# Kernel optimization log

Measured on AMD Instinct MI355X. Metric: run time of the kernel, lower is better.

The kernel has to match this reference:

```python
import jax, jax.numpy as jnp
import numpy as np

HID = 2880
NQ = 64
NKV = 8
HD = 64
THETA = 150000.0
WINDOW = 128
S = 8192


def _rope(x, positions):
    # x: [S, H, D]; half-split (rotate_half) convention
    d = x.shape[-1]
    inv_freq = 1.0 / (THETA ** (jnp.arange(0, d, 2, dtype=jnp.float32) / d))  # [D/2]
    ang = positions.astype(jnp.float32)[:, None] * inv_freq[None, :]          # [S, D/2]
    cos = jnp.cos(ang)[:, None, :]
    sin = jnp.sin(ang)[:, None, :]
    x1, x2 = jnp.split(x, 2, axis=-1)
    return jnp.concatenate([x1 * cos - x2 * sin, x2 * cos + x1 * sin], axis=-1)


def setup_inputs() -> dict:
    key = jax.random.key(0)
    ks = jax.random.split(key, 12)
    sd = 0.02
    return {
        "hidden": jax.random.normal(ks[0], (S, HID), dtype=jnp.float32),
        "positions": jnp.arange(S, dtype=jnp.int64) if jax.config.jax_enable_x64 else jnp.arange(S, dtype=jnp.int32),
        "Wq": jax.random.normal(ks[1], (HID, NQ * HD), dtype=jnp.float32) * sd,
        "bq": jax.random.normal(ks[2], (NQ * HD,), dtype=jnp.float32) * sd,
        "Wk": jax.random.normal(ks[3], (HID, NKV * HD), dtype=jnp.float32) * sd,
        "bk": jax.random.normal(ks[4], (NKV * HD,), dtype=jnp.float32) * sd,
        "Wv": jax.random.normal(ks[5], (HID, NKV * HD), dtype=jnp.float32) * sd,
        "bv": jax.random.normal(ks[6], (NKV * HD,), dtype=jnp.float32) * sd,
        "Wo": jax.random.normal(ks[7], (NQ * HD, HID), dtype=jnp.float32) * sd,
        "bo": jax.random.normal(ks[8], (HID,), dtype=jnp.float32) * sd,
    }


def _attention(hidden, positions, Wq, bq, Wk, bk, Wv, bv, Wo, bo):
    n_tok = hidden.shape[0]
    q = (hidden @ Wq + bq).reshape(n_tok, NQ, HD)
    k = (hidden @ Wk + bk).reshape(n_tok, NKV, HD)
    v = (hidden @ Wv + bv).reshape(n_tok, NKV, HD)
    q = _rope(q, positions)
    k = _rope(k, positions)

    # Blocked sliding-window causal attention (window == block size W).
    W = WINDOW
    nb = n_tok // W
    group = NQ // NKV
    qb = q.reshape(nb, W, NQ, HD)
    kb = k.reshape(nb, W, NKV, HD)
    vb = v.reshape(nb, W, NKV, HD)
    # each query block attends to its own block plus the previous one (2W keys)
    k_prev = jnp.concatenate([jnp.zeros_like(kb[:1]), kb[:-1]], axis=0)
    v_prev = jnp.concatenate([jnp.zeros_like(vb[:1]), vb[:-1]], axis=0)
    k_ctx = jnp.concatenate([k_prev, kb], axis=1)   # [nb, 2W, NKV, HD]
    v_ctx = jnp.concatenate([v_prev, vb], axis=1)
    # GQA: repeat KV heads to match query heads
    k_ctx = jnp.repeat(k_ctx, group, axis=2)        # [nb, 2W, NQ, HD]
    v_ctx = jnp.repeat(v_ctx, group, axis=2)

    scale = 1.0 / np.sqrt(HD)
    scores = jnp.einsum('bqhd,bkhd->bhqk', qb, k_ctx) * scale  # [nb, NQ, W, 2W]

    qi = jnp.arange(W)[:, None]            # local query pos
    ki = jnp.arange(2 * W)[None, :]        # local key pos within context
    diff = qi - ki + W                     # i - j (global)
    band = (diff >= 0) & (diff < WINDOW)   # causal + window
    kpos = jnp.arange(nb)[:, None, None] * W + ki[None] - W  # global key pos
    mask = band[None] & (kpos >= 0)        # [nb, W, 2W]

    neg = jnp.finfo(scores.dtype).min
    scores = jnp.where(mask[:, None, :, :], scores, neg)
    p = jax.nn.softmax(scores, axis=-1)
    attn = jnp.einsum('bhqk,bkhd->bqhd', p, v_ctx)  # [nb, W, NQ, HD]
    attn = attn.reshape(n_tok, NQ * HD)
    return attn @ Wo + bo


def reference(hidden, positions, Wq, bq, Wk, bk, Wv, bv, Wo, bo):
    return _attention(hidden, positions, Wq, bq, Wk, bk, Wv, bv, Wo, bo)
```

## Files before the change

### kernel.cpp

```cpp
#include <hip/hip_runtime.h>
#include <stdint.h>

#define S_TOK 8192
#define HID 2880
#define NQ 64
#define NKV 8
#define HD 64
#define QKV_N 5120
#define NO_PAD 2944

typedef __attribute__((ext_vector_type(8))) __bf16 bf16x8;
typedef __attribute__((ext_vector_type(4))) float f32x4;

__device__ __forceinline__ unsigned short f2bf(float f) {
  unsigned int u = __builtin_bit_cast(unsigned int, f);
  u += 0x7fff + ((u >> 16) & 1);
  return (unsigned short)(u >> 16);
}
__device__ __forceinline__ float bf2f(unsigned short h) {
  unsigned int u = ((unsigned int)h) << 16;
  return __builtin_bit_cast(float, u);
}

__device__ __forceinline__ void async_lds16(const void* g, void* l) {
  __builtin_amdgcn_global_load_lds(
      (const __attribute__((address_space(1))) unsigned int*)g,
      (__attribute__((address_space(3))) unsigned int*)l, 16, 0, 0);
}

__device__ __forceinline__ void wg_barrier() {
  asm volatile("" ::: "memory");
  __builtin_amdgcn_s_barrier();
  asm volatile("" ::: "memory");
}

__global__ __launch_bounds__(256) void cvt_bf16_kernel(
    const float* __restrict__ src, unsigned short* __restrict__ dst) {
  size_t i = ((size_t)blockIdx.x * 256 + threadIdx.x) * 8;
  float4 a = *(const float4*)(src + i);
  float4 b = *(const float4*)(src + i + 4);
  union { unsigned short u[8]; uint4 v; } o;
  o.u[0] = f2bf(a.x); o.u[1] = f2bf(a.y); o.u[2] = f2bf(a.z); o.u[3] = f2bf(a.w);
  o.u[4] = f2bf(b.x); o.u[5] = f2bf(b.y); o.u[6] = f2bf(b.z); o.u[7] = f2bf(b.w);
  *(uint4*)(dst + i) = o.v;
}

__global__ __launch_bounds__(256) void transpose_cvt(
    const float* __restrict__ src, unsigned short* __restrict__ dst,
    int R, int C, int rowOff) {
  __shared__ float tile[32][33];
  int tx = threadIdx.x, ty = threadIdx.y;
  int c0 = blockIdx.x * 32, r0 = blockIdx.y * 32;
#pragma unroll
  for (int i = 0; i < 4; ++i)
    tile[ty + i * 8][tx] = src[(size_t)(r0 + ty + i * 8) * C + c0 + tx];
  __syncthreads();
#pragma unroll
  for (int i = 0; i < 4; ++i)
    dst[(size_t)(c0 + ty + i * 8 + rowOff) * R + r0 + tx] = f2bf(tile[tx][ty + i * 8]);
}

__global__ __launch_bounds__(256) void rope_kernel(
    unsigned short* __restrict__ qkv, const int* __restrict__ positions) {
  int gid = blockIdx.x * 256 + threadIdx.x;
  int d = gid & 31;
  int rest = gid >> 5;
  int head = rest % 72;
  int t = rest / 72;
  unsigned short* p = qkv + (size_t)t * QKV_N + head * 64;
  float x1 = bf2f(p[d]);
  float x2 = bf2f(p[d + 32]);
  float pos = (float)positions[t];
  float inv = exp2f(-0.5373313430f * (float)d);
  float ang = pos * inv;
  float s = sinf(ang), c = cosf(ang);
  p[d] = f2bf(x1 * c - x2 * s);
  p[d + 32] = f2bf(x2 * c + x1 * s);
}

template <int MODE>
__global__ __launch_bounds__(512, 2) void gemm256(
    const unsigned short* __restrict__ A, const unsigned short* __restrict__ BT,
    void* __restrict__ Cout, int K, int NT,
    const float* __restrict__ b0, const float* __restrict__ b1,
    const float* __restrict__ b2) {
  __shared__ unsigned short lds[3 * 24576];
  const int tid = threadIdx.x;
  const int lane = tid & 63;
  const int wid = tid >> 6;
  const int wy = wid >> 2, wx = wid & 3;
  const int l15 = lane & 15, l4 = lane >> 4;
  const int m0 = blockIdx.y * 256, n0 = blockIdx.x * 128;

  const unsigned short* Ag = A + (size_t)m0 * K;
  const unsigned short* Bg = BT + (size_t)n0 * K;

  f32x4 acc[8][2];
#pragma unroll
  for (int m = 0; m < 8; ++m)
#pragma unroll
    for (int n = 0; n < 2; ++n)
#pragma unroll
      for (int r = 0; r < 4; ++r) acc[m][n][r] = 0.f;

  auto stageA = [&](int t, int buf) {
    unsigned short* dst = lds + buf * 24576;
    const unsigned short* G = Ag + t * 64;
#pragma unroll
    for (int rd = 0; rd < 4; ++rd) {
      int s = tid + rd * 512;
      int row = s >> 3;
      int g = (s & 7) ^ (row & 7);
      async_lds16(G + (size_t)row * K + g * 8, &dst[s * 8]);
    }
  };
  auto stageB = [&](int t, int buf) {
    unsigned short* dst = lds + buf * 24576 + 16384;
    const unsigned short* G = Bg + t * 64;
#pragma unroll
    for (int rd = 0; rd < 2; ++rd) {
      int s = tid + rd * 512;
      int row = s >> 3;
      int g = (s & 7) ^ (row & 7);
      async_lds16(G + (size_t)row * K + g * 8, &dst[s * 8]);
    }
  };

  stageA(0, 0); stageB(0, 0);
  stageA(1, 1); stageB(1, 1);
  asm volatile("s_waitcnt vmcnt(6)" ::: "memory");
  wg_barrier();

  int cur = 0, nxt = 2;
  for (int t = 0; t < NT; ++t) {
    const unsigned short* As = lds + cur * 24576;
    const unsigned short* Bs = As + 16384;
    bf16x8 bfrag[2][2], af0[4][2], af1[4][2];

#pragma unroll
    for (int n = 0; n < 2; ++n)
#pragma unroll
      for (int ks = 0; ks < 2; ++ks) {
        int row = wx * 32 + n * 16 + l15;
        int ch = (ks * 4 + l4) ^ (row & 7);
        bfrag[n][ks] = *(const bf16x8*)&Bs[row * 64 + ch * 8];
      }
#pragma unroll
    for (int m = 0; m < 4; ++m)
#pragma unroll
      for (int ks = 0; ks < 2; ++ks) {
        int row = wy * 128 + m * 16 + l15;
        int ch = (ks * 4 + l4) ^ (row & 7);
        af0[m][ks] = *(const bf16x8*)&As[row * 64 + ch * 8];
      }
    if (t + 2 < NT) stageA(t + 2, nxt);
    wg_barrier();
    asm volatile("s_waitcnt lgkmcnt(0)" ::: "memory");
    __builtin_amdgcn_sched_barrier(0);
    __builtin_amdgcn_s_setprio(1);
#pragma unroll
    for (int m = 0; m < 4; ++m)
#pragma unroll
      for (int n = 0; n < 2; ++n)
#pragma unroll
        for (int ks = 0; ks < 2; ++ks)
          acc[m][n] = __builtin_amdgcn_mfma_f32_16x16x32_bf16(
              af0[m][ks], bfrag[n][ks], acc[m][n], 0, 0, 0);
    __builtin_amdgcn_s_setprio(0);
    wg_barrier();

#pragma unroll
    for (int m = 0; m < 4; ++m)
#pragma unroll
      for (int ks = 0; ks < 2; ++ks) {
        int row = wy * 128 + (m + 4) * 16 + l15;
        int ch = (ks * 4 + l4) ^ (row & 7);
        af1[m][ks] = *(const bf16x8*)&As[row * 64 + ch * 8];
      }
    if (t + 2 < NT) stageB(t + 2, nxt);
    wg_barrier();
    asm volatile("s_waitcnt lgkmcnt(0)" ::: "memory");
    __builtin_amdgcn_sched_barrier(0);
    __builtin_amdgcn_s_setprio(1);
#pragma unroll
    for (int m = 0; m < 4; ++m)
#pragma unroll
      for (int n = 0; n < 2; ++n)
#pragma unroll
        for (int ks = 0; ks < 2; ++ks)
          acc[m + 4][n] = __builtin_amdgcn_mfma_f32_16x16x32_bf16(
              af1[m][ks], bfrag[n][ks], acc[m + 4][n], 0, 0, 0);
    __builtin_amdgcn_s_setprio(0);
    if (t + 2 < NT) { asm volatile("s_waitcnt vmcnt(6)" ::: "memory"); }
    else            { asm volatile("s_waitcnt vmcnt(0)" ::: "memory"); }
    wg_barrier();
    cur = (cur == 2) ? 0 : cur + 1;
    nxt = (nxt == 2) ? 0 : nxt + 1;
  }
  __syncthreads();

  if (MODE == 0) {
    unsigned short* ldsC = lds;
#pragma unroll
    for (int n = 0; n < 2; ++n) {
      int col = wx * 32 + n * 16 + l15;
      int gcol = n0 + col;
      float bias = (gcol < 4096) ? b0[gcol]
                                 : (gcol < 4608 ? b1[gcol - 4096] : b2[gcol - 4608]);
#pragma unroll
      for (int m = 0; m < 8; ++m)
#pragma unroll
        for (int r = 0; r < 4; ++r) {
          int row = wy * 128 + m * 16 + l4 * 4 + r;
          ldsC[row * 136 + col] = f2bf(acc[m][n][r] + bias);
        }
    }
    __syncthreads();
    unsigned short* C16 = (unsigned short*)Cout;
#pragma unroll
    for (int i = 0; i < 8; ++i) {
      int s = tid + i * 512;
      int row = s >> 4;
      int cc = (s & 15) * 8;
      *(uint4*)(C16 + (size_t)(m0 + row) * QKV_N + n0 + cc) =
          *(const uint4*)&ldsC[row * 136 + cc];
    }
  } else {
    float* Cf = (float*)Cout;
#pragma unroll
    for (int n = 0; n < 2; ++n) {
      int gcol = n0 + wx * 32 + n * 16 + l15;
      if (gcol < HID) {
        float bias = b0[gcol];
#pragma unroll
        for (int m = 0; m < 8; ++m)
#pragma unroll
          for (int r = 0; r < 4; ++r) {
            int row = m0 + wy * 128 + m * 16 + l4 * 4 + r;
            Cf[(size_t)row * HID + gcol] = acc[m][n][r] + bias;
          }
      }
    }
  }
}

__global__ __launch_bounds__(256) void attn_kernel(
    const unsigned short* __restrict__ qkv, unsigned short* __restrict__ attn) {
  __shared__ unsigned short Qs[64 * 72];
  __shared__ unsigned short Ks[192 * 72];
  __shared__ unsigned short VTs[64 * 200];

  const int tid = threadIdx.x;
  const int B = blockIdx.x;
  const int h = blockIdx.y;
  const int hk = h >> 3;
  const int wave = tid >> 6, lane = tid & 63;
  const int quad = lane >> 4, ml = lane & 15;

#pragma unroll
  for (int it = 0; it < 2; ++it) {
    int s = tid + it * 256;
    int row = s >> 3, c = (s & 7) << 3;
    *(uint4*)&Qs[row * 72 + c] =
        *(const uint4*)(qkv + (size_t)(B * 64 + row) * QKV_N + h * 64 + c);
  }
#pragma unroll
  for (int it = 0; it < 6; ++it) {
    int s = tid + it * 256;
    int j = s >> 3, c = (s & 7) << 3;
    int tk = B * 64 - 128 + j;
    uint4 kv = make_uint4(0, 0, 0, 0), vv = make_uint4(0, 0, 0, 0);
    if (tk >= 0) {
      kv = *(const uint4*)(qkv + (size_t)tk * QKV_N + 4096 + hk * 64 + c);
      vv = *(const uint4*)(qkv + (size_t)tk * QKV_N + 4608 + hk * 64 + c);
    }
    *(uint4*)&Ks[j * 72 + c] = kv;
    union { uint4 q; unsigned short u[8]; } vu;
    vu.q = vv;
#pragma unroll
    for (int e = 0; e < 8; ++e) VTs[(c + e) * 200 + j] = vu.u[e];
  }
  __syncthreads();

  f32x4 zero = {0.f, 0.f, 0.f, 0.f};
  f32x4 sc[12];
#pragma unroll
  for (int jn = 0; jn < 12; ++jn) sc[jn] = zero;
#pragma unroll
  for (int kk = 0; kk < 2; ++kk) {
    bf16x8 af = *(const bf16x8*)&Qs[(wave * 16 + ml) * 72 + kk * 32 + quad * 8];
#pragma unroll
    for (int jn = 0; jn < 12; ++jn) {
      bf16x8 bfr = *(const bf16x8*)&Ks[(jn * 16 + ml) * 72 + kk * 32 + quad * 8];
      sc[jn] = __builtin_amdgcn_mfma_f32_16x16x32_bf16(af, bfr, sc[jn], 0, 0, 0);
    }
  }

  const float NEG = -3.0e38f;
  float mx[4], sm[4];
#pragma unroll
  for (int r = 0; r < 4; ++r) mx[r] = NEG;
#pragma unroll
  for (int jn = 0; jn < 12; ++jn) {
    int j = jn * 16 + ml;
#pragma unroll
    for (int r = 0; r < 4; ++r) {
      int i = wave * 16 + quad * 4 + r;
      bool valid = (j > i) && (j <= i + 128) && (B * 64 + j - 128 >= 0);
      float v = valid ? sc[jn][r] * 0.125f : NEG;
      sc[jn][r] = v;
      mx[r] = fmaxf(mx[r], v);
    }
  }
#pragma unroll
  for (int r = 0; r < 4; ++r) {
#pragma unroll
    for (int off = 1; off < 16; off <<= 1)
      mx[r] = fmaxf(mx[r], __shfl_xor(mx[r], off, 64));
    sm[r] = 0.f;
  }
#pragma unroll
  for (int jn = 0; jn < 12; ++jn) {
#pragma unroll
    for (int r = 0; r < 4; ++r) {
      float p = expf(sc[jn][r] - mx[r]);
      sc[jn][r] = p;
      sm[r] += p;
    }
  }
#pragma unroll
  for (int r = 0; r < 4; ++r) {
#pragma unroll
    for (int off = 1; off < 16; off <<= 1) sm[r] += __shfl_xor(sm[r], off, 64);
    sm[r] = 1.0f / sm[r];
  }
  __syncthreads();

  unsigned short* P = Ks;
#pragma unroll
  for (int jn = 0; jn < 12; ++jn) {
#pragma unroll
    for (int r = 0; r < 4; ++r)
      P[(wave * 16 + quad * 4 + r) * 200 + jn * 16 + ml] = f2bf(sc[jn][r] * sm[r]);
  }
  __syncthreads();

  f32x4 ov[4];
#pragma unroll
  for (int jn = 0; jn < 4; ++jn) ov[jn] = zero;
#pragma unroll
  for (int ks = 0; ks < 6; ++ks) {
    bf16x8 af = *(const bf16x8*)&P[(wave * 16 + ml) * 200 + ks * 32 + quad * 8];
#pragma unroll
    for (int jn = 0; jn < 4; ++jn) {
      bf16x8 bfr = *(const bf16x8*)&VTs[(jn * 16 + ml) * 200 + ks * 32 + quad * 8];
      ov[jn] = __builtin_amdgcn_mfma_f32_16x16x32_bf16(af, bfr, ov[jn], 0, 0, 0);
    }
  }
#pragma unroll
  for (int jn = 0; jn < 4; ++jn) {
#pragma unroll
    for (int r = 0; r < 4; ++r) {
      int row = B * 64 + wave * 16 + quad * 4 + r;
      attn[(size_t)row * 4096 + h * 64 + jn * 16 + ml] = f2bf(ov[jn][r]);
    }
  }
}

extern "C" void kernel_launch(void* const* d_in, const int* in_sizes, int n_in,
                              void* d_out, int out_size, void* d_ws, size_t ws_size,
                              hipStream_t stream) {
  const float* hidden = (const float*)d_in[0];
  const int* positions = (const int*)d_in[1];
  const float* Wq = (const float*)d_in[2];
  const float* bq = (const float*)d_in[3];
  const float* Wk = (const float*)d_in[4];
  const float* bk = (const float*)d_in[5];
  const float* Wv = (const float*)d_in[6];
  const float* bv = (const float*)d_in[7];
  const float* Wo = (const float*)d_in[8];
  const float* bo = (const float*)d_in[9];
  float* out = (float*)d_out;

  char* ws = (char*)d_ws;
  unsigned short* A_h   = (unsigned short*)(ws);
  unsigned short* BTqkv = (unsigned short*)(ws + 47185920);
  unsigned short* qkv   = (unsigned short*)(ws + 76677120);
  unsigned short* BTo   = (unsigned short*)(ws + 160563200);
  unsigned short* attn  = (unsigned short*)(ws);

  cvt_bf16_kernel<<<11520, 256, 0, stream>>>(hidden, A_h);
  dim3 tb(32, 8);
  transpose_cvt<<<dim3(128, 90), tb, 0, stream>>>(Wq, BTqkv, HID, 4096, 0);
  transpose_cvt<<<dim3(16, 90), tb, 0, stream>>>(Wk, BTqkv, HID, 512, 4096);
  transpose_cvt<<<dim3(16, 90), tb, 0, stream>>>(Wv, BTqkv, HID, 512, 4608);
  transpose_cvt<<<dim3(90, 128), tb, 0, stream>>>(Wo, BTo, 4096, HID, 0);
  hipMemsetAsync(BTo + (size_t)HID * 4096, 0, (size_t)(NO_PAD - HID) * 4096 * 2, stream);

  gemm256<0><<<dim3(QKV_N / 128, S_TOK / 256), 512, 0, stream>>>(
      A_h, BTqkv, qkv, HID, HID / 64, bq, bk, bv);
  rope_kernel<<<73728, 256, 0, stream>>>(qkv, positions);
  attn_kernel<<<dim3(S_TOK / 64, NQ), 256, 0, stream>>>(qkv, attn);
  gemm256<1><<<dim3(NO_PAD / 128, S_TOK / 256), 512, 0, stream>>>(
      attn, BTo, out, 4096, 4096 / 64, bo, nullptr, nullptr);
}
```

Before: 904.4 us.

## Enlarge GEMM tiles to 256x256 with split-K-half double buffering and grid swizzle

Reworks the bf16 GEMM from 256x128 to 256x256 output tiles. The LDS pipeline changes from three 64-wide K buffers to two buffers, each split into two 32-wide K halves. A 1D grid with an XCD-style block swizzle and a clamped B row index replaces the 2D grid, and the epilogue writes in two halves through LDS. The goal is more reuse per loaded A/B byte and better L2 locality. The cost is twice the accumulator registers, which could reduce occupancy or cause spills, plus wasted work in the padded final N tile for the output projection (2944 vs 3072).

```diff
diff --git a/kernel.cpp b/kernel.cpp
--- a/kernel.cpp
+++ b/kernel.cpp
@@ -33,6 +33,13 @@
   __builtin_amdgcn_s_barrier();
   asm volatile("" ::: "memory");
 }
+
+#define VMCNT(n) asm volatile("s_waitcnt vmcnt(" #n ")" ::: "memory")
+#define LGKM0                                            \
+  do {                                                   \
+    asm volatile("s_waitcnt lgkmcnt(0)" ::: "memory");   \
+    __builtin_amdgcn_sched_barrier(0);                   \
+  } while (0)
 
 __global__ __launch_bounds__(256) void cvt_bf16_kernel(
     const float* __restrict__ src, unsigned short* __restrict__ dst) {
@@ -81,155 +88,173 @@
 template <int MODE>
 __global__ __launch_bounds__(512, 2) void gemm256(
     const unsigned short* __restrict__ A, const unsigned short* __restrict__ BT,
-    void* __restrict__ Cout, int K, int NT,
+    void* __restrict__ Cout, int K, int NT, int nbClamp, int gx,
     const float* __restrict__ b0, const float* __restrict__ b1,
     const float* __restrict__ b2) {
-  __shared__ unsigned short lds[3 * 24576];
+  __shared__ unsigned short lds[65536];
   const int tid = threadIdx.x;
   const int lane = tid & 63;
   const int wid = tid >> 6;
   const int wy = wid >> 2, wx = wid & 3;
   const int l15 = lane & 15, l4 = lane >> 4;
-  const int m0 = blockIdx.y * 256, n0 = blockIdx.x * 128;
+  const int psw = l4 ^ ((l15 >> 1) & 3);
+
+  int nwg = gridDim.x;
+  int bid = blockIdx.x;
+  int swz = (bid & 7) * (nwg >> 3) + (bid >> 3);
+  int bx = swz % gx, by = swz / gx;
+  const int m0 = by * 256, n0 = bx * 256;
 
   const unsigned short* Ag = A + (size_t)m0 * K;
-  const unsigned short* Bg = BT + (size_t)n0 * K;
-
-  f32x4 acc[8][2];
+
+  const int row0 = tid >> 2;
+  const int gsw = (tid & 3) ^ ((tid >> 3) & 3);
+
+  auto stageA = [&](int t, int kh, int buf) {
+    const unsigned short* G = Ag + t * 64 + kh * 32;
+    unsigned short* D = &lds[buf * 32768 + kh * 8192];
+#pragma unroll
+    for (int rd = 0; rd < 2; ++rd) {
+      int row = row0 + rd * 128;
+      async_lds16(G + (size_t)row * K + gsw * 8, D + (tid + rd * 512) * 8);
+    }
+  };
+  auto stageB = [&](int t, int kh, int buf) {
+    int koff = t * 64 + kh * 32;
+    unsigned short* D = &lds[buf * 32768 + 16384 + kh * 8192];
+#pragma unroll
+    for (int rd = 0; rd < 2; ++rd) {
+      int gr = n0 + row0 + rd * 128;
+      gr = gr > nbClamp ? nbClamp : gr;
+      async_lds16(BT + (size_t)gr * K + koff + gsw * 8, D + (tid + rd * 512) * 8);
+    }
+  };
+
+  f32x4 acc[8][4];
 #pragma unroll
   for (int m = 0; m < 8; ++m)
 #pragma unroll
-    for (int n = 0; n < 2; ++n)
+    for (int n = 0; n < 4; ++n)
 #pragma unroll
       for (int r = 0; r < 4; ++r) acc[m][n][r] = 0.f;
 
-  auto stageA = [&](int t, int buf) {
-    unsigned short* dst = lds + buf * 24576;
-    const unsigned short* G = Ag + t * 64;
-#pragma unroll
-    for (int rd = 0; rd < 4; ++rd) {
-      int s = tid + rd * 512;
-      int row = s >> 3;
-      int g = (s & 7) ^ (row & 7);
-      async_lds16(G + (size_t)row * K + g * 8, &dst[s * 8]);
-    }
-  };
-  auto stageB = [&](int t, int buf) {
-    unsigned short* dst = lds + buf * 24576 + 16384;
-    const unsigned short* G = Bg + t * 64;
-#pragma unroll
-    for (int rd = 0; rd < 2; ++rd) {
-      int s = tid + rd * 512;
-      int row = s >> 3;
-      int g = (s & 7) ^ (row & 7);
-      async_lds16(G + (size_t)row * K + g * 8, &dst[s * 8]);
-    }
-  };
-
-  stageA(0, 0); stageB(0, 0);
-  stageA(1, 1); stageB(1, 1);
-  asm volatile("s_waitcnt vmcnt(6)" ::: "memory");
-  wg_barrier();
-
-  int cur = 0, nxt = 2;
+  stageB(0, 0, 0); stageA(0, 0, 0); stageB(0, 1, 0); stageA(0, 1, 0);
+  stageB(1, 0, 1); stageA(1, 0, 1); stageB(1, 1, 1);
+
+  bf16x8 aq[4], bq[4];
   for (int t = 0; t < NT; ++t) {
-    const unsigned short* As = lds + cur * 24576;
-    const unsigned short* Bs = As + 16384;
-    bf16x8 bfrag[2][2], af0[4][2], af1[4][2];
-
-#pragma unroll
-    for (int n = 0; n < 2; ++n)
-#pragma unroll
-      for (int ks = 0; ks < 2; ++ks) {
-        int row = wx * 32 + n * 16 + l15;
-        int ch = (ks * 4 + l4) ^ (row & 7);
-        bfrag[n][ks] = *(const bf16x8*)&Bs[row * 64 + ch * 8];
+    const int cur = t & 1;
+    const unsigned short* Ab0 = &lds[cur * 32768];
+    const unsigned short* Bb0 = Ab0 + 16384;
+    const unsigned short* Ab1 = Ab0 + 8192;
+    const unsigned short* Bb1 = Bb0 + 8192;
+
+    if (t + 1 < NT) { VMCNT(10); } else { VMCNT(4); }
+    wg_barrier();
+    if (t + 1 < NT) stageA(t + 1, 1, cur ^ 1);
+#pragma unroll
+    for (int n = 0; n < 4; ++n)
+      bq[n] = *(const bf16x8*)&Bb0[(wx * 64 + n * 16 + l15) * 32 + psw * 8];
+#pragma unroll
+    for (int mi = 0; mi < 4; ++mi)
+      aq[mi] = *(const bf16x8*)&Ab0[(wy * 128 + mi * 16 + l15) * 32 + psw * 8];
+    LGKM0;
+    __builtin_amdgcn_s_setprio(1);
+#pragma unroll
+    for (int mi = 0; mi < 4; ++mi)
+#pragma unroll
+      for (int n = 0; n < 4; ++n)
+        acc[mi][n] = __builtin_amdgcn_mfma_f32_16x16x32_bf16(
+            aq[mi], bq[n], acc[mi][n], 0, 0, 0);
+    __builtin_amdgcn_s_setprio(0);
+
+    wg_barrier();
+    if (t + 2 < NT) stageB(t + 2, 0, cur);
+#pragma unroll
+    for (int mi = 0; mi < 4; ++mi)
+      aq[mi] = *(const bf16x8*)&Ab0[(wy * 128 + (mi + 4) * 16 + l15) * 32 + psw * 8];
+    LGKM0;
+    __builtin_amdgcn_s_setprio(1);
+#pragma unroll
+    for (int mi = 0; mi < 4; ++mi)
+#pragma unroll
+      for (int n = 0; n < 4; ++n)
+        acc[mi + 4][n] = __builtin_amdgcn_mfma_f32_16x16x32_bf16(
+            aq[mi], bq[n], acc[mi + 4][n], 0, 0, 0);
+    __builtin_amdgcn_s_setprio(0);
+
+    if (t + 2 < NT) { VMCNT(10); }
+    else if (t + 1 < NT) { VMCNT(8); }
+    else { VMCNT(0); }
+    wg_barrier();
+    if (t + 2 < NT) stageA(t + 2, 0, cur);
+#pragma unroll
+    for (int n = 0; n < 4; ++n)
+      bq[n] = *(const bf16x8*)&Bb1[(wx * 64 + n * 16 + l15) * 32 + psw * 8];
+#pragma unroll
+    for (int mi = 0; mi < 4; ++mi)
+      aq[mi] = *(const bf16x8*)&Ab1[(wy * 128 + mi * 16 + l15) * 32 + psw * 8];
+    LGKM0;
+    __builtin_amdgcn_s_setprio(1);
+#pragma unroll
+    for (int mi = 0; mi < 4; ++mi)
+#pragma unroll
+      for (int n = 0; n < 4; ++n)
+        acc[mi][n] = __builtin_amdgcn_mfma_f32_16x16x32_bf16(
+            aq[mi], bq[n], acc[mi][n], 0, 0, 0);
+    __builtin_amdgcn_s_setprio(0);
+
+    wg_barrier();
+    if (t + 2 < NT) stageB(t + 2, 1, cur);
+#pragma unroll
+    for (int mi = 0; mi < 4; ++mi)
+      aq[mi] = *(const bf16x8*)&Ab1[(wy * 128 + (mi + 4) * 16 + l15) * 32 + psw * 8];
+    LGKM0;
+    __builtin_amdgcn_s_setprio(1);
+#pragma unroll
+    for (int mi = 0; mi < 4; ++mi)
+#pragma unroll
+      for (int n = 0; n < 4; ++n)
+        acc[mi + 4][n] = __builtin_amdgcn_mfma_f32_16x16x32_bf16(
+            aq[mi], bq[n], acc[mi + 4][n], 0, 0, 0);
+    __builtin_amdgcn_s_setprio(0);
+  }
+  __syncthreads();
+
+  if (MODE == 0) {
+    unsigned short* C16 = (unsigned short*)Cout;
+    unsigned short* ldsC = lds;
+#pragma unroll
+    for (int h = 0; h < 2; ++h) {
+      if (wy == h) {
+#pragma unroll
+        for (int n = 0; n < 4; ++n) {
+          int col = wx * 64 + n * 16 + l15;
+          int gcol = n0 + col;
+          float bias = (gcol < 4096) ? b0[gcol]
+                                     : (gcol < 4608 ? b1[gcol - 4096] : b2[gcol - 4608]);
+#pragma unroll
+          for (int m = 0; m < 8; ++m)
+#pragma unroll
+            for (int r = 0; r < 4; ++r)
+              ldsC[(m * 16 + l4 * 4 + r) * 264 + col] = f2bf(acc[m][n][r] + bias);
+        }
       }
-#pragma unroll
-    for (int m = 0; m < 4; ++m)
-#pragma unroll
-      for (int ks = 0; ks < 2; ++ks) {
-        int row = wy * 128 + m * 16 + l15;
-        int ch = (ks * 4 + l4) ^ (row & 7);
-        af0[m][ks] = *(const bf16x8*)&As[row * 64 + ch * 8];
+      __syncthreads();
+#pragma unroll
+      for (int it = 0; it < 8; ++it) {
+        int s = tid + it * 512;
+        int row = s >> 5, c8 = (s & 31) * 8;
+        *(uint4*)(C16 + (size_t)(m0 + h * 128 + row) * QKV_N + n0 + c8) =
+            *(const uint4*)&ldsC[row * 264 + c8];
       }
-    if (t + 2 < NT) stageA(t + 2, nxt);
-    wg_barrier();
-    asm volatile("s_waitcnt lgkmcnt(0)" ::: "memory");
-    __builtin_amdgcn_sched_barrier(0);
-    __builtin_amdgcn_s_setprio(1);
-#pragma unroll
-    for (int m = 0; m < 4; ++m)
-#pragma unroll
-      for (int n = 0; n < 2; ++n)
-#pragma unroll
-        for (int ks = 0; ks < 2; ++ks)
-          acc[m][n] = __builtin_amdgcn_mfma_f32_16x16x32_bf16(
-              af0[m][ks], bfrag[n][ks], acc[m][n], 0, 0, 0);
-    __builtin_amdgcn_s_setprio(0);
-    wg_barrier();
-
-#pragma unroll
-    for (int m = 0; m < 4; ++m)
-#pragma unroll
-      for (int ks = 0; ks < 2; ++ks) {
-        int row = wy * 128 + (m + 4) * 16 + l15;
-        int ch = (ks * 4 + l4) ^ (row & 7);
-        af1[m][ks] = *(const bf16x8*)&As[row * 64 + ch * 8];
-      }
-    if (t + 2 < NT) stageB(t + 2, nxt);
-    wg_barrier();
-    asm volatile("s_waitcnt lgkmcnt(0)" ::: "memory");
-    __builtin_amdgcn_sched_barrier(0);
-    __builtin_amdgcn_s_setprio(1);
-#pragma unroll
-    for (int m = 0; m < 4; ++m)
-#pragma unroll
-      for (int n = 0; n < 2; ++n)
-#pragma unroll
-        for (int ks = 0; ks < 2; ++ks)
-          acc[m + 4][n] = __builtin_amdgcn_mfma_f32_16x16x32_bf16(
-              af1[m][ks], bfrag[n][ks], acc[m + 4][n], 0, 0, 0);
-    __builtin_amdgcn_s_setprio(0);
-    if (t + 2 < NT) { asm volatile("s_waitcnt vmcnt(6)" ::: "memory"); }
-    else            { asm volatile("s_waitcnt vmcnt(0)" ::: "memory"); }
-    wg_barrier();
-    cur = (cur == 2) ? 0 : cur + 1;
-    nxt = (nxt == 2) ? 0 : nxt + 1;
-  }
-  __syncthreads();
-
-  if (MODE == 0) {
-    unsigned short* ldsC = lds;
-#pragma unroll
-    for (int n = 0; n < 2; ++n) {
-      int col = wx * 32 + n * 16 + l15;
-      int gcol = n0 + col;
-      float bias = (gcol < 4096) ? b0[gcol]
-                                 : (gcol < 4608 ? b1[gcol - 4096] : b2[gcol - 4608]);
-#pragma unroll
-      for (int m = 0; m < 8; ++m)
-#pragma unroll
-        for (int r = 0; r < 4; ++r) {
-          int row = wy * 128 + m * 16 + l4 * 4 + r;
-          ldsC[row * 136 + col] = f2bf(acc[m][n][r] + bias);
-        }
-    }
-    __syncthreads();
-    unsigned short* C16 = (unsigned short*)Cout;
-#pragma unroll
-    for (int i = 0; i < 8; ++i) {
-      int s = tid + i * 512;
-      int row = s >> 4;
-      int cc = (s & 15) * 8;
-      *(uint4*)(C16 + (size_t)(m0 + row) * QKV_N + n0 + cc) =
-          *(const uint4*)&ldsC[row * 136 + cc];
+      if (h == 0) __syncthreads();
     }
   } else {
     float* Cf = (float*)Cout;
 #pragma unroll
-    for (int n = 0; n < 2; ++n) {
-      int gcol = n0 + wx * 32 + n * 16 + l15;
+    for (int n = 0; n < 4; ++n) {
+      int gcol = n0 + wx * 64 + n * 16 + l15;
       if (gcol < HID) {
         float bias = b0[gcol];
 #pragma unroll
@@ -397,10 +422,10 @@
   transpose_cvt<<<dim3(90, 128), tb, 0, stream>>>(Wo, BTo, 4096, HID, 0);
   hipMemsetAsync(BTo + (size_t)HID * 4096, 0, (size_t)(NO_PAD - HID) * 4096 * 2, stream);
 
-  gemm256<0><<<dim3(QKV_N / 128, S_TOK / 256), 512, 0, stream>>>(
-      A_h, BTqkv, qkv, HID, HID / 64, bq, bk, bv);
+  gemm256<0><<<dim3(20 * 32), 512, 0, stream>>>(
+      A_h, BTqkv, qkv, HID, 45, QKV_N - 1, 20, bq, bk, bv);
   rope_kernel<<<73728, 256, 0, stream>>>(qkv, positions);
   attn_kernel<<<dim3(S_TOK / 64, NQ), 256, 0, stream>>>(qkv, attn);
-  gemm256<1><<<dim3(NO_PAD / 128, S_TOK / 256), 512, 0, stream>>>(
-      attn, BTo, out, 4096, 4096 / 64, bo, nullptr, nullptr);
-}
+  gemm256<1><<<dim3(12 * 32), 512, 0, stream>>>(
+      attn, BTo, out, 4096, 64, NO_PAD - 1, 12, bo, nullptr, nullptr);
+}
```

Measured after the change: 934.5 us. 1.03x slower.
